# Performance work log

Measured on AMD Instinct MI355X. Metric: run time of the kernel, lower is better.

Reference implementation:

```python
import jax, jax.numpy as jnp
import numpy as np

B, L, H, D = 2, 2048, 16, 64


def setup_inputs() -> dict:
    key = jax.random.key(0)
    k1, k2, k3, k4 = jax.random.split(key, 4)
    query_states = jax.random.normal(k1, (B, L, H, D), dtype=jnp.float32)
    key_states = jax.random.normal(k2, (B, L, H, D), dtype=jnp.float32)
    # per-head linear feature maps (LinearFeatureMap parameters)
    Wq = jax.random.normal(k3, (H, D, D), dtype=jnp.float32)
    Wk = jax.random.normal(k4, (H, D, D), dtype=jnp.float32)
    return {"query_states": query_states, "key_states": key_states, "Wq": Wq, "Wk": Wk}


def reference(query_states, key_states, Wq, Wk):
    # per-head linear feature map: [B,L,H,D] x [H,D,E] -> [B,L,H,E]
    q = jnp.einsum('blhd,hde->blhe', query_states, Wq)
    k = jnp.einsum('blhd,hde->blhe', key_states, Wk)
    # kernelized attention scores: [B,H,L,S]
    attn = jnp.einsum('blhd,bshd->bhls', q, k)
    # sum-normalization over keys (non-softmax normalizer)
    attn = attn / jnp.sum(attn, axis=-1, keepdims=True)
    return attn
```

## Files before the change

### kernel.cpp

```cpp
#include <hip/hip_runtime.h>
#include <stdint.h>

#define NB 2
#define NL 2048
#define NH 16
#define ND 64

typedef __attribute__((ext_vector_type(8))) short short8;
typedef __attribute__((ext_vector_type(4))) float f32x4;
typedef __attribute__((ext_vector_type(4))) unsigned short ushort4v;

__device__ __forceinline__ unsigned short f2bf_rne(float x) {
    union { float f; unsigned int u; } v; v.f = x;
    unsigned int r = v.u + 0x7fffu + ((v.u >> 16) & 1u);
    return (unsigned short)(r >> 16);
}
__device__ __forceinline__ float bf2f(unsigned short b) {
    union { unsigned int u; float f; } v; v.u = ((unsigned int)b) << 16;
    return v.f;
}

__global__ __launch_bounds__(256) void pre_kernel(const float* __restrict__ query,
                                                  const float* __restrict__ key,
                                                  const float* __restrict__ Wq,
                                                  const float* __restrict__ Wk,
                                                  unsigned short* __restrict__ qbh,
                                                  unsigned short* __restrict__ qbl,
                                                  unsigned short* __restrict__ kbh,
                                                  unsigned short* __restrict__ kbl,
                                                  double* __restrict__ part) {
    __shared__ __align__(16) char lds_raw[16384 + 34816];
    const int blk = blockIdx.x;
    const int t = threadIdx.x;

    if (blk < 1024) {
        const bool isq = blk < 512;
        const int pb = isq ? blk : blk - 512;
        const float* x = isq ? query : key;
        const float* W = isq ? Wq : Wk;
        unsigned short* ph = isq ? qbh : kbh;
        unsigned short* pl = isq ? qbl : kbl;
        float* Wlds = (float*)lds_raw;
        float* xs = (float*)(lds_raw + 16384);

        const int lc = pb & 15;
        const int h = (pb >> 4) & 15;
        const int b = pb >> 8;
        const int l0 = lc * 128;

        {
            const float4* src = (const float4*)(W + (size_t)h * ND * ND);
#pragma unroll
            for (int i = 0; i < 4; ++i)
                ((float4*)Wlds)[t + 256 * i] = src[t + 256 * i];
        }
        {
#pragma unroll
            for (int i = 0; i < 8; ++i) {
                const int idx = t + 256 * i;
                const int r = idx >> 4, c = idx & 15;
                const float4 v = *(const float4*)(x + (((size_t)b * NL + l0 + r) * NH + h) * ND + c * 4);
                *(float4*)&xs[r * 68 + c * 4] = v;
            }
        }
        __syncthreads();

        const int e4 = (t & 15) * 4;
        const int rg = t >> 4;
        float acc[8][4] = {};
        for (int d = 0; d < ND; ++d) {
            const float4 w4 = *(const float4*)&Wlds[d * ND + e4];
#pragma unroll
            for (int it = 0; it < 8; ++it) {
                const float xv = xs[(rg + it * 16) * 68 + d];
                acc[it][0] += xv * w4.x; acc[it][1] += xv * w4.y;
                acc[it][2] += xv * w4.z; acc[it][3] += xv * w4.w;
            }
        }

        unsigned short* phh = ph + ((size_t)(b * NH + h) * NL + l0) * ND;
        unsigned short* pll = pl + ((size_t)(b * NH + h) * NL + l0) * ND;
#pragma unroll
        for (int it = 0; it < 8; ++it) {
            const int r = rg + it * 16;
            const int ep = e4 ^ ((r & 7) << 3);
            ushort4v hv, lv;
#pragma unroll
            for (int j = 0; j < 4; ++j) {
                const unsigned short hb = f2bf_rne(acc[it][j]);
                hv[j] = hb;
                lv[j] = f2bf_rne(acc[it][j] - bf2f(hb));
            }
            *(ushort4v*)&phh[(size_t)r * ND + ep] = hv;
            *(ushort4v*)&pll[(size_t)r * ND + ep] = lv;
        }
    } else {
        double (*red)[64] = (double(*)[64])lds_raw;
        const int blk2 = blk - 1024;
        const int chunk = blk2 & 15, bh = blk2 >> 4;
        const int b = bh >> 4, h = bh & 15;
        const int e = t & 63, sub = t >> 6;
        const float* base = key + ((size_t)b * NL * NH + h) * ND + e;
        double acc = 0.0;
        const int s0 = chunk * 128 + sub * 32;
        for (int s = s0; s < s0 + 32; ++s)
            acc += (double)base[(size_t)s * (NH * ND)];
        red[sub][e] = acc;
        __syncthreads();
        if (t < 64) {
            const double s2 = red[0][t] + red[1][t] + red[2][t] + red[3][t];
            part[(size_t)blk2 * 64 + t] = s2;
        }
    }
}

__global__ __launch_bounds__(256) void den_kernel(const float* __restrict__ xq,
                                                  const double* __restrict__ part,
                                                  const float* __restrict__ Wq,
                                                  const float* __restrict__ Wk,
                                                  float* __restrict__ invden) {
    __shared__ double xs[ND], ks[ND], vs[ND];
    const int bh = blockIdx.x;
    const int b = bh >> 4, h = bh & 15;
    const int t = threadIdx.x;
    if (t < 64) {
        double a = 0.0;
#pragma unroll
        for (int c = 0; c < 16; ++c) a += part[((size_t)bh * 16 + c) * 64 + t];
        xs[t] = a;
    }
    __syncthreads();
    if (t < 64) {
        double acc = 0.0;
        const float* wk = Wk + (size_t)h * ND * ND + t;
        for (int d = 0; d < ND; ++d) acc += xs[d] * (double)wk[(size_t)d * ND];
        ks[t] = acc;
    }
    __syncthreads();
    if (t < 64) {
        double acc = 0.0;
        const float* wq = Wq + (size_t)h * ND * ND + (size_t)t * ND;
        for (int e = 0; e < ND; ++e) acc += (double)wq[e] * ks[e];
        vs[t] = acc;
    }
    __syncthreads();
    const int l = blockIdx.y * 256 + t;
    const float* xp = xq + (((size_t)b * NL + l) * NH + h) * ND;
    double acc = 0.0;
#pragma unroll 8
    for (int d = 0; d < ND; ++d) acc += (double)xp[d] * vs[d];
    invden[(size_t)bh * NL + l] = (float)(1.0 / acc);
}

__global__ __launch_bounds__(512, 1) void attn_kernel(const unsigned short* __restrict__ qbh,
                                                      const unsigned short* __restrict__ qbl,
                                                      const unsigned short* __restrict__ kbh,
                                                      const unsigned short* __restrict__ kbl,
                                                      const float* __restrict__ invden,
                                                      float* __restrict__ out) {
    __shared__ unsigned short kwbuf[8][2][2][32 * 64];
    const int strip = blockIdx.x;
    const int bh = blockIdx.y;
    const int t = threadIdx.x;
    const int w = t >> 6, ln = t & 63;
    const int fr = ln & 15, g = ln >> 4;
    const int swz = (fr & 7) << 4;
    const int cofs0 = (g << 4) ^ swz;
    const int cofs1 = (64 | (g << 4)) ^ swz;

    const size_t pan = (size_t)bh * NL * ND;
    const unsigned short* kh_p = kbh + pan;
    const unsigned short* kl_p = kbl + pan;
    const char* qh_pb = (const char*)(qbh + pan);
    const char* ql_pb = (const char*)(qbl + pan);
    const int lbase = strip * 256 + w * 32;

    short8 qf00, qf01, qf10, qf11, qg00, qg01, qg10, qg11;
    {
        const size_t r0 = (size_t)(lbase + fr) * 128;
        const size_t r1 = (size_t)(lbase + 16 + fr) * 128;
        qf00 = *(const short8*)(qh_pb + r0 + cofs0);
        qf01 = *(const short8*)(qh_pb + r0 + cofs1);
        qf10 = *(const short8*)(ql_pb + r0 + cofs0);
        qf11 = *(const short8*)(ql_pb + r0 + cofs1);
        qg00 = *(const short8*)(qh_pb + r1 + cofs0);
        qg01 = *(const short8*)(qh_pb + r1 + cofs1);
        qg10 = *(const short8*)(ql_pb + r1 + cofs0);
        qg11 = *(const short8*)(ql_pb + r1 + cofs1);
    }
    const float inv0 = invden[(size_t)bh * NL + lbase + fr];
    const float inv1 = invden[(size_t)bh * NL + lbase + 16 + fr];
    asm volatile("s_waitcnt vmcnt(0)" ::: "memory");
    __builtin_amdgcn_sched_barrier(0);

#define STAGE(c, buf)                                                                               \
    {                                                                                               \
        _Pragma("unroll")                                                                           \
        for (int u = 0; u < 4; ++u) {                                                               \
            __builtin_amdgcn_global_load_lds(                                                       \
                (const __attribute__((address_space(1))) unsigned int*)(kh_p + (size_t)(c) * 2048 + u * 512 + ln * 8), \
                (__attribute__((address_space(3))) unsigned int*)(&kwbuf[w][buf][0][u * 512]), 16, 0, 0); \
        }                                                                                           \
        _Pragma("unroll")                                                                           \
        for (int u = 0; u < 4; ++u) {                                                               \
            __builtin_amdgcn_global_load_lds(                                                       \
                (const __attribute__((address_space(1))) unsigned int*)(kl_p + (size_t)(c) * 2048 + u * 512 + ln * 8), \
                (__attribute__((address_space(3))) unsigned int*)(&kwbuf[w][buf][1][u * 512]), 16, 0, 0); \
        }                                                                                           \
    }

#define COMPUTE(c, b)                                                                               \
    {                                                                                               \
        const char* kh_b = (const char*)&kwbuf[w][b][0][0];                                         \
        const char* kl_b = (const char*)&kwbuf[w][b][1][0];                                         \
        _Pragma("unroll")                                                                           \
        for (int is = 0; is < 2; ++is) {                                                            \
            const int soff = (is * 16 + fr) * 128;                                                  \
            const short8 kh0 = *(const short8*)(kh_b + soff + cofs0);                               \
            const short8 kh1 = *(const short8*)(kh_b + soff + cofs1);                               \
            const short8 kl0 = *(const short8*)(kl_b + soff + cofs0);                               \
            const short8 kl1 = *(const short8*)(kl_b + soff + cofs1);                               \
            {                                                                                       \
                f32x4 a = (f32x4){0.f, 0.f, 0.f, 0.f};                                              \
                a = __builtin_amdgcn_mfma_f32_16x16x32_bf16(kh0, qf00, a, 0, 0, 0);                 \
                a = __builtin_amdgcn_mfma_f32_16x16x32_bf16(kh0, qf10, a, 0, 0, 0);                 \
                a = __builtin_amdgcn_mfma_f32_16x16x32_bf16(kl0, qf00, a, 0, 0, 0);                 \
                a = __builtin_amdgcn_mfma_f32_16x16x32_bf16(kh1, qf01, a, 0, 0, 0);                 \
                a = __builtin_amdgcn_mfma_f32_16x16x32_bf16(kh1, qf11, a, 0, 0, 0);                 \
                a = __builtin_amdgcn_mfma_f32_16x16x32_bf16(kl1, qf01, a, 0, 0, 0);                 \
                f32x4 vv = a;                                                                       \
                vv[0] *= inv0; vv[1] *= inv0; vv[2] *= inv0; vv[3] *= inv0;                         \
                *(f32x4*)(out + ((size_t)bh * NL + lbase + fr) * NL + (c) * 32 + is * 16 + g * 4) = vv; \
            }                                                                                       \
            {                                                                                       \
                f32x4 a = (f32x4){0.f, 0.f, 0.f, 0.f};                                              \
                a = __builtin_amdgcn_mfma_f32_16x16x32_bf16(kh0, qg00, a, 0, 0, 0);                 \
                a = __builtin_amdgcn_mfma_f32_16x16x32_bf16(kh0, qg10, a, 0, 0, 0);                 \
                a = __builtin_amdgcn_mfma_f32_16x16x32_bf16(kl0, qg00, a, 0, 0, 0);                 \
                a = __builtin_amdgcn_mfma_f32_16x16x32_bf16(kh1, qg01, a, 0, 0, 0);                 \
                a = __builtin_amdgcn_mfma_f32_16x16x32_bf16(kh1, qg11, a, 0, 0, 0);                 \
                a = __builtin_amdgcn_mfma_f32_16x16x32_bf16(kl1, qg01, a, 0, 0, 0);                 \
                f32x4 vv = a;                                                                       \
                vv[0] *= inv1; vv[1] *= inv1; vv[2] *= inv1; vv[3] *= inv1;                         \
                *(f32x4*)(out + ((size_t)bh * NL + lbase + 16 + fr) * NL + (c) * 32 + is * 16 + g * 4) = vv; \
            }                                                                                       \
        }                                                                                           \
    }

#define LDS_FENCE()                                         \
    asm volatile("s_waitcnt lgkmcnt(0)" ::: "memory");      \
    __builtin_amdgcn_sched_barrier(0)

    STAGE(0, 0);
    STAGE(1, 1);

    asm volatile("s_waitcnt vmcnt(8)" ::: "memory");
    __builtin_amdgcn_sched_barrier(0);
    COMPUTE(0, 0);
    LDS_FENCE();
    STAGE(2, 0);

    for (int c = 1; c <= 61; ++c) {
        asm volatile("s_waitcnt vmcnt(12)" ::: "memory");
        __builtin_amdgcn_sched_barrier(0);
        const int b = c & 1;
        COMPUTE(c, b);
        LDS_FENCE();
        STAGE(c + 2, b);
    }

    asm volatile("s_waitcnt vmcnt(12)" ::: "memory");
    __builtin_amdgcn_sched_barrier(0);
    COMPUTE(62, 0);

    asm volatile("s_waitcnt vmcnt(4)" ::: "memory");
    __builtin_amdgcn_sched_barrier(0);
    COMPUTE(63, 1);

#undef STAGE
#undef COMPUTE
#undef LDS_FENCE
}

extern "C" void kernel_launch(void* const* d_in, const int* in_sizes, int n_in,
                              void* d_out, int out_size, void* d_ws, size_t ws_size,
                              hipStream_t stream) {
    const float* query = (const float*)d_in[0];
    const float* key   = (const float*)d_in[1];
    const float* Wq    = (const float*)d_in[2];
    const float* Wk    = (const float*)d_in[3];
    float* out = (float*)d_out;

    const size_t npan = (size_t)NB * NH * NL * ND;
    char* ws = (char*)d_ws;
    unsigned short* qbh = (unsigned short*)(ws);
    unsigned short* qbl = (unsigned short*)(ws + 1 * npan * 2);
    unsigned short* kbh = (unsigned short*)(ws + 2 * npan * 2);
    unsigned short* kbl = (unsigned short*)(ws + 3 * npan * 2);
    double* part  = (double*)(ws + 4 * npan * 2);
    float* invden = (float*)(ws + 4 * npan * 2 + 262144);

    pre_kernel<<<1536, 256, 0, stream>>>(query, key, Wq, Wk, qbh, qbl, kbh, kbl, part);
    den_kernel<<<dim3(NB * NH, NL / 256), 256, 0, stream>>>(query, part, Wq, Wk, invden);
    attn_kernel<<<dim3(8, NB * NH), 512, 0, stream>>>(qbh, qbl, kbh, kbl, invden, out);
}
```

Before: 184.0 us.

## Stage attention output tiles through LDS for full-row coalesced global stores

Each warp now writes its scaled MFMA results into a swizzled LDS output buffer and, every four 16-key chunks, flushes 32 rows by 64 columns with stores that cover 256 contiguous bytes per row. Before, each lane stored a 16-byte fragment scattered across 16 rows. The K staging chunk is halved to 16 keys and the pipeline is re-timed with new vmcnt thresholds. The goal is better write coalescing on the large output, at the cost of extra LDS traffic, an extra lgkm fence per flush, and more shared memory.

```diff
diff --git a/kernel.cpp b/kernel.cpp
--- a/kernel.cpp
+++ b/kernel.cpp
@@ -158,7 +158,8 @@
                                                       const unsigned short* __restrict__ kbl,
                                                       const float* __restrict__ invden,
                                                       float* __restrict__ out) {
-    __shared__ unsigned short kwbuf[8][2][2][32 * 64];
+    __shared__ unsigned short kwbuf[8][2][2][1024];
+    __shared__ f32x4 obuf[8][512];
     const int strip = blockIdx.x;
     const int bh = blockIdx.y;
     const int t = threadIdx.x;
@@ -196,90 +197,105 @@
 #define STAGE(c, buf)                                                                               \
     {                                                                                               \
         _Pragma("unroll")                                                                           \
-        for (int u = 0; u < 4; ++u) {                                                               \
+        for (int u = 0; u < 2; ++u) {                                                               \
             __builtin_amdgcn_global_load_lds(                                                       \
-                (const __attribute__((address_space(1))) unsigned int*)(kh_p + (size_t)(c) * 2048 + u * 512 + ln * 8), \
+                (const __attribute__((address_space(1))) unsigned int*)(kh_p + (size_t)(c) * 1024 + u * 512 + ln * 8), \
                 (__attribute__((address_space(3))) unsigned int*)(&kwbuf[w][buf][0][u * 512]), 16, 0, 0); \
         }                                                                                           \
         _Pragma("unroll")                                                                           \
-        for (int u = 0; u < 4; ++u) {                                                               \
+        for (int u = 0; u < 2; ++u) {                                                               \
             __builtin_amdgcn_global_load_lds(                                                       \
-                (const __attribute__((address_space(1))) unsigned int*)(kl_p + (size_t)(c) * 2048 + u * 512 + ln * 8), \
+                (const __attribute__((address_space(1))) unsigned int*)(kl_p + (size_t)(c) * 1024 + u * 512 + ln * 8), \
                 (__attribute__((address_space(3))) unsigned int*)(&kwbuf[w][buf][1][u * 512]), 16, 0, 0); \
         }                                                                                           \
     }
 
-#define COMPUTE(c, b)                                                                               \
+#define WAITN(n)                                            \
+    asm volatile("s_waitcnt vmcnt(" #n ")" ::: "memory");   \
+    __builtin_amdgcn_sched_barrier(0)
+
+#define LDS_FENCE()                                         \
+    asm volatile("s_waitcnt lgkmcnt(0)" ::: "memory");      \
+    __builtin_amdgcn_sched_barrier(0)
+
+#define COMPUTE(b, cc)                                                                              \
     {                                                                                               \
         const char* kh_b = (const char*)&kwbuf[w][b][0][0];                                         \
         const char* kl_b = (const char*)&kwbuf[w][b][1][0];                                         \
+        const int soff = fr * 128;                                                                  \
+        const short8 kh0 = *(const short8*)(kh_b + soff + cofs0);                                   \
+        const short8 kh1 = *(const short8*)(kh_b + soff + cofs1);                                   \
+        const short8 kl0 = *(const short8*)(kl_b + soff + cofs0);                                   \
+        const short8 kl1 = *(const short8*)(kl_b + soff + cofs1);                                   \
+        {                                                                                           \
+            f32x4 a = (f32x4){0.f, 0.f, 0.f, 0.f};                                                  \
+            a = __builtin_amdgcn_mfma_f32_16x16x32_bf16(kh0, qf00, a, 0, 0, 0);                     \
+            a = __builtin_amdgcn_mfma_f32_16x16x32_bf16(kh0, qf10, a, 0, 0, 0);                     \
+            a = __builtin_amdgcn_mfma_f32_16x16x32_bf16(kl0, qf00, a, 0, 0, 0);                     \
+            a = __builtin_amdgcn_mfma_f32_16x16x32_bf16(kh1, qf01, a, 0, 0, 0);                     \
+            a = __builtin_amdgcn_mfma_f32_16x16x32_bf16(kh1, qf11, a, 0, 0, 0);                     \
+            a = __builtin_amdgcn_mfma_f32_16x16x32_bf16(kl1, qf01, a, 0, 0, 0);                     \
+            a[0] *= inv0; a[1] *= inv0; a[2] *= inv0; a[3] *= inv0;                                 \
+            obuf[w][fr * 16 + (((cc) * 4 + g) ^ fr)] = a;                                           \
+        }                                                                                           \
+        {                                                                                           \
+            f32x4 a = (f32x4){0.f, 0.f, 0.f, 0.f};                                                  \
+            a = __builtin_amdgcn_mfma_f32_16x16x32_bf16(kh0, qg00, a, 0, 0, 0);                     \
+            a = __builtin_amdgcn_mfma_f32_16x16x32_bf16(kh0, qg10, a, 0, 0, 0);                     \
+            a = __builtin_amdgcn_mfma_f32_16x16x32_bf16(kl0, qg00, a, 0, 0, 0);                     \
+            a = __builtin_amdgcn_mfma_f32_16x16x32_bf16(kh1, qg01, a, 0, 0, 0);                     \
+            a = __builtin_amdgcn_mfma_f32_16x16x32_bf16(kh1, qg11, a, 0, 0, 0);                     \
+            a = __builtin_amdgcn_mfma_f32_16x16x32_bf16(kl1, qg01, a, 0, 0, 0);                     \
+            a[0] *= inv1; a[1] *= inv1; a[2] *= inv1; a[3] *= inv1;                                 \
+            obuf[w][(16 + fr) * 16 + (((cc) * 4 + g) ^ fr)] = a;                                    \
+        }                                                                                           \
+    }
+
+#define FLUSH(c4)                                                                                   \
+    {                                                                                               \
+        f32x4 ov[8];                                                                                \
         _Pragma("unroll")                                                                           \
-        for (int is = 0; is < 2; ++is) {                                                            \
-            const int soff = (is * 16 + fr) * 128;                                                  \
-            const short8 kh0 = *(const short8*)(kh_b + soff + cofs0);                               \
-            const short8 kh1 = *(const short8*)(kh_b + soff + cofs1);                               \
-            const short8 kl0 = *(const short8*)(kl_b + soff + cofs0);                               \
-            const short8 kl1 = *(const short8*)(kl_b + soff + cofs1);                               \
-            {                                                                                       \
-                f32x4 a = (f32x4){0.f, 0.f, 0.f, 0.f};                                              \
-                a = __builtin_amdgcn_mfma_f32_16x16x32_bf16(kh0, qf00, a, 0, 0, 0);                 \
-                a = __builtin_amdgcn_mfma_f32_16x16x32_bf16(kh0, qf10, a, 0, 0, 0);                 \
-                a = __builtin_amdgcn_mfma_f32_16x16x32_bf16(kl0, qf00, a, 0, 0, 0);                 \
-                a = __builtin_amdgcn_mfma_f32_16x16x32_bf16(kh1, qf01, a, 0, 0, 0);                 \
-                a = __builtin_amdgcn_mfma_f32_16x16x32_bf16(kh1, qf11, a, 0, 0, 0);                 \
-                a = __builtin_amdgcn_mfma_f32_16x16x32_bf16(kl1, qf01, a, 0, 0, 0);                 \
-                f32x4 vv = a;                                                                       \
-                vv[0] *= inv0; vv[1] *= inv0; vv[2] *= inv0; vv[3] *= inv0;                         \
-                *(f32x4*)(out + ((size_t)bh * NL + lbase + fr) * NL + (c) * 32 + is * 16 + g * 4) = vv; \
-            }                                                                                       \
-            {                                                                                       \
-                f32x4 a = (f32x4){0.f, 0.f, 0.f, 0.f};                                              \
-                a = __builtin_amdgcn_mfma_f32_16x16x32_bf16(kh0, qg00, a, 0, 0, 0);                 \
-                a = __builtin_amdgcn_mfma_f32_16x16x32_bf16(kh0, qg10, a, 0, 0, 0);                 \
-                a = __builtin_amdgcn_mfma_f32_16x16x32_bf16(kl0, qg00, a, 0, 0, 0);                 \
-                a = __builtin_amdgcn_mfma_f32_16x16x32_bf16(kh1, qg01, a, 0, 0, 0);                 \
-                a = __builtin_amdgcn_mfma_f32_16x16x32_bf16(kh1, qg11, a, 0, 0, 0);                 \
-                a = __builtin_amdgcn_mfma_f32_16x16x32_bf16(kl1, qg01, a, 0, 0, 0);                 \
-                f32x4 vv = a;                                                                       \
-                vv[0] *= inv1; vv[1] *= inv1; vv[2] *= inv1; vv[3] *= inv1;                         \
-                *(f32x4*)(out + ((size_t)bh * NL + lbase + 16 + fr) * NL + (c) * 32 + is * 16 + g * 4) = vv; \
-            }                                                                                       \
-        }                                                                                           \
-    }
-
-#define LDS_FENCE()                                         \
-    asm volatile("s_waitcnt lgkmcnt(0)" ::: "memory");      \
-    __builtin_amdgcn_sched_barrier(0)
+        for (int k8 = 0; k8 < 8; ++k8) {                                                            \
+            const int row = k8 * 4 + (ln >> 4);                                                     \
+            ov[k8] = obuf[w][row * 16 + ((ln & 15) ^ (row & 15))];                                  \
+        }                                                                                           \
+        LDS_FENCE();                                                                                \
+        _Pragma("unroll")                                                                           \
+        for (int k8 = 0; k8 < 8; ++k8) {                                                            \
+            const int row = k8 * 4 + (ln >> 4);                                                     \
+            *(f32x4*)(out + ((size_t)bh * NL + lbase + row) * NL + (c4) * 64 + (ln & 15) * 4) = ov[k8]; \
+        }                                                                                           \
+    }
 
     STAGE(0, 0);
     STAGE(1, 1);
 
-    asm volatile("s_waitcnt vmcnt(8)" ::: "memory");
-    __builtin_amdgcn_sched_barrier(0);
-    COMPUTE(0, 0);
-    LDS_FENCE();
-    STAGE(2, 0);
-
-    for (int c = 1; c <= 61; ++c) {
-        asm volatile("s_waitcnt vmcnt(12)" ::: "memory");
-        __builtin_amdgcn_sched_barrier(0);
-        const int b = c & 1;
-        COMPUTE(c, b);
-        LDS_FENCE();
-        STAGE(c + 2, b);
-    }
-
-    asm volatile("s_waitcnt vmcnt(12)" ::: "memory");
-    __builtin_amdgcn_sched_barrier(0);
-    COMPUTE(62, 0);
-
-    asm volatile("s_waitcnt vmcnt(4)" ::: "memory");
-    __builtin_amdgcn_sched_barrier(0);
-    COMPUTE(63, 1);
+    WAITN(4); COMPUTE(0, 0); LDS_FENCE(); STAGE(2, 0);
+    WAITN(4); COMPUTE(1, 1); LDS_FENCE(); STAGE(3, 1);
+    WAITN(4); COMPUTE(0, 2); LDS_FENCE(); STAGE(4, 0);
+    WAITN(4); COMPUTE(1, 3); LDS_FENCE(); STAGE(5, 1);
+    FLUSH(0);
+
+    for (int c4 = 1; c4 <= 30; ++c4) {
+        const int c = c4 * 4;
+        WAITN(12); COMPUTE(0, 0); LDS_FENCE(); STAGE(c + 2, 0);
+        WAITN(12); COMPUTE(1, 1); LDS_FENCE(); STAGE(c + 3, 1);
+        WAITN(4);  COMPUTE(0, 2); LDS_FENCE(); STAGE(c + 4, 0);
+        WAITN(4);  COMPUTE(1, 3); LDS_FENCE(); STAGE(c + 5, 1);
+        FLUSH(c4);
+    }
+
+    WAITN(12); COMPUTE(0, 0); LDS_FENCE(); STAGE(126, 0);
+    WAITN(12); COMPUTE(1, 1); LDS_FENCE(); STAGE(127, 1);
+    WAITN(4);  COMPUTE(0, 2); LDS_FENCE();
+    WAITN(0);  COMPUTE(1, 3); LDS_FENCE();
+    FLUSH(31);
 
 #undef STAGE
+#undef WAITN
+#undef LDS_FENCE
 #undef COMPUTE
-#undef LDS_FENCE
+#undef FLUSH
 }
 
 extern "C" void kernel_launch(void* const* d_in, const int* in_sizes, int n_in,
```

New measurement: 178.9 us. 1.03x faster.
